# Optimization experiments

Measured on AMD Instinct MI355X. Metric: run time of the kernel, lower is better.

Reference implementation:

```python
import jax, jax.numpy as jnp
import numpy as np

B, C, V, K, H, W = 1, 3, 9, 8, 512, 512


def setup_inputs() -> dict:
    key = jax.random.key(0)
    k0, k1 = jax.random.split(key, 2)
    x = jax.random.normal(k0, (B, C, K, H, W), jnp.float32)          # FDL layers (spatial)
    y_views = jax.random.normal(k1, (B, C, V, H, W), jnp.float32)    # observed views (spatial)
    g = jnp.arange(3, dtype=jnp.float32) - 1.0                       # 3x3 camera grid positions
    uu, vv = jnp.meshgrid(g, g, indexing='ij')
    u = uu.reshape(-1)
    v = vv.reshape(-1)
    d = jnp.linspace(-2.0, 2.0, K).astype(jnp.float32)               # d_fdl disparities
    rho = jnp.full((1,), 0.3, jnp.float32)
    return {"x": x, "y_views": y_views, "u": u, "v": v, "d": d, "rho": rho}


def _pack_half_spectrum(Xf, x_c, y_c, n_proc):
    # [..., H, W] -> transpose to [..., W, H], center-roll so zero freq is at (x_c-1, y_c-1),
    # flatten x-major, keep the non-redundant half spectrum (first n_proc entries).
    Xt = jnp.swapaxes(Xf, -1, -2)
    Xt = jnp.roll(Xt, shift=(x_c - 1, y_c - 1), axis=(-2, -1))
    sh = Xt.shape
    return Xt.reshape(sh[:-2] + (sh[-2] * sh[-1],))[..., :n_proc]


def reference(x, y_views, u, v, d, rho):
    Bn, Cn, Kn = x.shape[0], x.shape[1], x.shape[2]
    Hn, Wn = x.shape[-2], x.shape[-1]
    rho = rho.reshape(())
    x_c = (Wn + 2) // 2                      # ceil((W+1)/2)
    y_c = (Hn + 2) // 2
    n_proc = Hn * (x_c - 1) + y_c            # half-spectrum size
    e0 = 1 - Hn % 2
    e1 = 1 - Wn % 2

    X = jnp.fft.fft2(x)                      # [B,C,K,H,W] complex64
    Y = jnp.fft.fft2(y_views)                # [B,C,V,H,W] complex64
    Xp = jnp.moveaxis(_pack_half_spectrum(X, x_c, y_c, n_proc), 2, 3) * rho   # [B,C,F,K]
    Yp = jnp.moveaxis(_pack_half_spectrum(Y, x_c, y_c, n_proc), 2, 3)         # [B,C,F,V]

    # centered angular frequency grids, flattened x-major to match packing order
    wx = (jnp.arange(Wn, dtype=jnp.float32) - (x_c - 1)) * (2.0 * np.pi / Wn)
    wy = (jnp.arange(Hn, dtype=jnp.float32) - (y_c - 1)) * (2.0 * np.pi / Hn)
    wx_f = jnp.repeat(wx, Hn)[:n_proc]       # [F]
    wy_f = jnp.tile(wy, Wn)[:n_proc]         # [F]

    # FDL data matrix A[f,v,k] = exp(i * d_k * (u_v*wx_f + v_v*wy_f))
    shift = u[None, :] * wx_f[:, None] + v[None, :] * wy_f[:, None]   # [F,V]
    A = jnp.exp(1j * shift[:, :, None] * d[None, None, :])            # [F,V,K] complex64
    Ah = jnp.conj(A)
    ATA = jnp.einsum('fvk,fvl->fkl', Ah, A)                           # [F,K,K]
    ATb = jnp.einsum('fvk,bcfv->bcfk', Ah, Yp)                        # [B,C,F,K]
    M = ATA + rho * jnp.eye(Kn, dtype=ATA.dtype)
    fdl = jnp.linalg.solve(M, (ATb + Xp)[..., None])[..., 0]          # [B,C,F,K]

    # pad redundant half with zeros, restore [B,C,K,H,W] layout
    fdl = jnp.pad(fdl, ((0, 0), (0, 0), (0, Hn * Wn - n_proc), (0, 0)))
    fdl = fdl.reshape(Bn, Cn, Wn, Hn, Kn).transpose(0, 1, 4, 3, 2)    # [B,C,K,H,W]

    # Hermitian (conjugate) symmetry reconstruction
    fdl = fdl.at[..., y_c:, x_c - 1:].set(jnp.conj(fdl[..., e0:y_c - 1, e1:x_c][..., ::-1, ::-1]))
    fdl = fdl.at[..., e0:y_c, x_c:].set(jnp.conj(fdl[..., y_c - 1:, e1:x_c - 1][..., ::-1, ::-1]))
    fdl = jnp.roll(fdl, shift=(1 - y_c, 1 - x_c), axis=(-2, -1))
    return jnp.fft.ifft2(fdl).real
```

## Files before the change

### kernel.cpp

```cpp
#include <hip/hip_runtime.h>
#include <math.h>

constexpr int N    = 512;
constexpr int LOGN = 9;
constexpr int NN   = N * N;
constexpr int CCH  = 3;
constexpr int KK   = 8;
constexpr int VV   = 9;
constexpr int FHALF = N * (N / 2) + (N / 2 + 1);
constexpr int NS   = 257;
constexpr float PI_F = 3.14159265358979323846f;

__device__ __forceinline__ float2 cmulf(float2 a, float2 b) {
    return make_float2(a.x * b.x - a.y * b.y, a.x * b.y + a.y * b.x);
}
__device__ __forceinline__ float2 cadd(float2 a, float2 b) { return make_float2(a.x + b.x, a.y + b.y); }
__device__ __forceinline__ float2 csub(float2 a, float2 b) { return make_float2(a.x - b.x, a.y - b.y); }

template<int SG>
__device__ __forceinline__ float2 cmuli(float2 z) {
    return (SG < 0) ? make_float2(z.y, -z.x) : make_float2(-z.y, z.x);
}

template<int SG>
__device__ __forceinline__ void dft8(float2 x[8]) {
    const float c = 0.70710678118654752440f;
    float2 a0 = cadd(x[0], x[4]), a1 = cadd(x[1], x[5]);
    float2 a2 = cadd(x[2], x[6]), a3 = cadd(x[3], x[7]);
    float2 d0 = csub(x[0], x[4]), d1 = csub(x[1], x[5]);
    float2 d2 = csub(x[2], x[6]), d3 = csub(x[3], x[7]);
    float2 b0 = d0;
    float2 b1 = cmulf(d1, make_float2(c, (float)SG * c));
    float2 b2 = cmuli<SG>(d2);
    float2 b3 = cmulf(d3, make_float2(-c, (float)SG * c));
    float2 aa0 = cadd(a0, a2), aa1 = cadd(a1, a3);
    float2 ab0 = csub(a0, a2), ab1 = cmuli<SG>(csub(a1, a3));
    float2 ba0 = cadd(b0, b2), ba1 = cadd(b1, b3);
    float2 bb0 = csub(b0, b2), bb1 = cmuli<SG>(csub(b1, b3));
    x[0] = cadd(aa0, aa1); x[4] = csub(aa0, aa1);
    x[2] = cadd(ab0, ab1); x[6] = csub(ab0, ab1);
    x[1] = cadd(ba0, ba1); x[5] = csub(ba0, ba1);
    x[3] = cadd(bb0, bb1); x[7] = csub(bb0, bb1);
}

__device__ __forceinline__ void twiddle8(float2 v[8], float base) {
    float sn, cs;
    __sincosf(base, &sn, &cs);
    float2 w1 = make_float2(cs, sn);
    float2 wk = w1;
    v[1] = cmulf(v[1], wk);
    #pragma unroll
    for (int k = 2; k < 8; ++k) { wk = cmulf(wk, w1); v[k] = cmulf(v[k], wk); }
}

template<int SG>
__device__ __forceinline__ void wave_fft512(float2 v[8], float* sre, float* sim,
                                            int t, int stride, int off) {
    int t1 = t >> 3, t0 = t & 7;
    dft8<SG>(v);
    twiddle8(v, (float)SG * (2.0f * PI_F / 512.0f) * (float)t);
    #pragma unroll
    for (int k = 0; k < 8; ++k) {
        int a = (68 * k + 8 * t1 + t0) * stride + off;
        sre[a] = v[k].x; sim[a] = v[k].y;
    }
    #pragma unroll
    for (int n = 0; n < 8; ++n) {
        int a = (68 * t1 + 8 * n + t0) * stride + off;
        v[n] = make_float2(sre[a], sim[a]);
    }
    dft8<SG>(v);
    twiddle8(v, (float)SG * (2.0f * PI_F / 64.0f) * (float)t0);
    #pragma unroll
    for (int k = 0; k < 8; ++k) {
        int a = (68 * t0 + 8 * k + t1) * stride + off;
        sre[a] = v[k].x; sim[a] = v[k].y;
    }
    #pragma unroll
    for (int n = 0; n < 8; ++n) {
        int a = (68 * n + 8 * t0 + t1) * stride + off;
        v[n] = make_float2(sre[a], sim[a]);
    }
    dft8<SG>(v);
}

__global__ __launch_bounds__(256) void k_fft_r2c_rows_pack_T(const float* __restrict__ inx,
                                                             const float* __restrict__ iny,
                                                             int nximg,
                                                             float2* __restrict__ outT) {
    __shared__ float ure[2313];
    __shared__ float uim[2313];
    int w = threadIdx.x >> 6, t = threadIdx.x & 63;
    int blk = blockIdx.x;
    int img = blk >> 6;
    int rowbase = (blk & 63) << 3;
    long long row0 = (long long)blk * 8 + 2 * w;
    long long xrows = (long long)nximg * N;
    const float* src0 = (row0 < xrows) ? (inx + row0 * N)
                                       : (iny + (row0 - xrows) * N);
    const float* src1 = src0 + N;
    float* sre = ure + w * 544;
    float* sim = uim + w * 544;
    float2 v[8];
    #pragma unroll
    for (int e = 0; e < 8; ++e) v[e] = make_float2(src0[t + 64 * e], src1[t + 64 * e]);
    wave_fft512<-1>(v, sre, sim, t, 1, 0);
    int kb = (t >> 3) + 8 * (t & 7);
    #pragma unroll
    for (int k0 = 0; k0 < 8; ++k0) {
        int p = kb + 64 * k0;
        sre[p] = v[k0].x; sim[p] = v[k0].y;
    }
    float2 r0v[4], r1v[4];
    #pragma unroll
    for (int k0 = 4; k0 < 8; ++k0) {
        int p  = kb + 64 * k0;
        int mp = 512 - p;
        float zmx = sre[mp], zmy = sim[mp];
        float2 Zp = v[k0];
        r0v[k0 - 4] = make_float2(0.5f * (Zp.x + zmx), 0.5f * (Zp.y - zmy));
        r1v[k0 - 4] = make_float2(0.5f * (Zp.y + zmy), 0.5f * (zmx - Zp.x));
    }
    float2 z0 = v[0];
    __syncthreads();
    #pragma unroll
    for (int k0 = 0; k0 < 4; ++k0) {
        int s = kb + 64 * k0;
        ure[s * 9 + 2 * w]     = r0v[k0].x; uim[s * 9 + 2 * w]     = r0v[k0].y;
        ure[s * 9 + 2 * w + 1] = r1v[k0].x; uim[s * 9 + 2 * w + 1] = r1v[k0].y;
    }
    if (t == 0) {
        ure[256 * 9 + 2 * w]     = z0.x; uim[256 * 9 + 2 * w]     = 0.0f;
        ure[256 * 9 + 2 * w + 1] = z0.y; uim[256 * 9 + 2 * w + 1] = 0.0f;
    }
    __syncthreads();
    float2* dst = outT + (long long)img * ((long long)NS * N);
    int tt = threadIdx.x;
    int r = tt & 7;
    #pragma unroll
    for (int j = 0; j < 8; ++j) {
        int s = j * 32 + (tt >> 3);
        dst[s * N + rowbase + r] = make_float2(ure[s * 9 + r], uim[s * 9 + r]);
    }
    if (tt < 8)
        dst[256 * N + rowbase + tt] = make_float2(ure[256 * 9 + tt], uim[256 * 9 + tt]);
}

__global__ __launch_bounds__(256) void k_fft_r2c_rows(const float* __restrict__ in,
                                                      float2* __restrict__ out) {
    __shared__ float sre[4][544];
    __shared__ float sim[4][544];
    int w = threadIdx.x >> 6, t = threadIdx.x & 63;
    long long grow = (long long)blockIdx.x * 4 + w;
    const float* src = in + grow * N;
    float2 v[8];
    #pragma unroll
    for (int e = 0; e < 8; ++e) v[e] = make_float2(src[t + 64 * e], 0.0f);
    wave_fft512<-1>(v, sre[w], sim[w], t, 1, 0);
    float2* dst = out + grow * N;
    int kb = (t >> 3) + 8 * (t & 7);
    #pragma unroll
    for (int k0 = 0; k0 < 8; ++k0) dst[kb + 64 * k0] = v[k0];
}

template<int SG>
__global__ __launch_bounds__(256) void k_fft_pairswap(float2* __restrict__ data,
                                                      float scale, int lex, int sex) {
    __shared__ float sre[4][544];
    __shared__ float sim[4][544];
    int w = threadIdx.x >> 6, t = threadIdx.x & 63;
    int b = blockIdx.x;
    long long imgBase = (long long)(b >> 7) * NN;
    int pa = (b & 127) << 1;
    int rowg = pa + (w & 1) + ((w >> 1) << 8);
    const float2* src = data + imgBase + (long long)rowg * N;
    float2 v[8];
    #pragma unroll
    for (int e = 0; e < 8; ++e) v[e] = src[t + 64 * (e ^ lex)];
    __syncthreads();
    wave_fft512<SG>(v, sre[w], sim[w], t, 1, 0);
    float2* dst = data + imgBase + (long long)(rowg ^ 256) * N;
    int kb = (t >> 3) + 8 * (t & 7);
    #pragma unroll
    for (int k0 = 0; k0 < 8; ++k0) {
        float2 z = v[k0];
        dst[kb + 64 * (k0 ^ sex)] = make_float2(z.x * scale, z.y * scale);
    }
}

__device__ __forceinline__ void accum_pair(float2 bacc[KK], float tr[KK], float s,
                                           float d0, float dlt, float2 Yp, float2 Yn) {
    float2 Sp = make_float2(Yp.x + Yn.x, Yp.y + Yn.y);
    float2 Dm = make_float2(Yp.x - Yn.x, Yp.y - Yn.y);
    float sn, cs;
    __sincosf(s * d0, &sn, &cs);  float2 p = make_float2(cs, sn);
    __sincosf(s * dlt, &sn, &cs); float2 q = make_float2(cs, sn);
    float2 w = q;
    #pragma unroll
    for (int k = 0; k < KK; ++k) {
        bacc[k].x += p.x * Sp.x + p.y * Dm.y;
        bacc[k].y += p.x * Sp.y - p.y * Dm.x;
        if (k < KK - 1) {
            p = cmulf(p, q);
            tr[k + 1] += 2.0f * w.x;
            w = cmulf(w, q);
        }
    }
}

__device__ __forceinline__ void solve_point(float2 bacc[KK], float tr[KK], float rho) {
    float diag = tr[0] + rho;
    float L[36], Li[KK];
    #pragma unroll
    for (int j = 0; j < KK; ++j) {
        float acc = diag;
        #pragma unroll
        for (int t = 0; t < j; ++t) { float l = L[(j * (j - 1)) / 2 + t]; acc -= l * l; }
        float dj = sqrtf(acc);
        float inv = 1.0f / dj;
        Li[j] = inv;
        #pragma unroll
        for (int i = j + 1; i < KK; ++i) {
            float a = tr[i - j];
            #pragma unroll
            for (int t = 0; t < j; ++t)
                a -= L[(i * (i - 1)) / 2 + t] * L[(j * (j - 1)) / 2 + t];
            L[(i * (i - 1)) / 2 + j] = a * inv;
        }
    }
    #pragma unroll
    for (int i = 0; i < KK; ++i) {
        float2 a = bacc[i];
        #pragma unroll
        for (int t = 0; t < i; ++t) {
            float l = L[(i * (i - 1)) / 2 + t];
            a.x -= l * bacc[t].x;
            a.y -= l * bacc[t].y;
        }
        bacc[i] = make_float2(a.x * Li[i], a.y * Li[i]);
    }
    #pragma unroll
    for (int i = KK - 1; i >= 0; --i) {
        float2 a = bacc[i];
        #pragma unroll
        for (int t = i + 1; t < KK; ++t) {
            float l = L[(t * (t - 1)) / 2 + i];
            a.x -= l * bacc[t].x;
            a.y -= l * bacc[t].y;
        }
        bacc[i] = make_float2(a.x * Li[i], a.y * Li[i]);
    }
}

__global__ __launch_bounds__(256) void k_fused_solve(const float2* __restrict__ Rt,
                                                     float2* __restrict__ P,
                                                     float2* __restrict__ S0,
                                                     int nximg,
                                                     const float* __restrict__ uu,
                                                     const float* __restrict__ vvp,
                                                     const float* __restrict__ dd,
                                                     const float* __restrict__ rhop) {
    __shared__ float2 buf[VV][N];
    __shared__ float fsre[4][544];
    __shared__ float fsim[4][544];
    int a  = blockIdx.x;
    int ch = blockIdx.y;
    int t  = threadIdx.x;
    int w = t >> 6, lane = t & 63;
    int kb = (lane >> 3) + 8 * (lane & 7);
    const long long LN = (long long)NS * N;

    {
        int ybase = nximg + ch * VV;
        #pragma unroll
        for (int rep = 0; rep < 3; ++rep) {
            int vimg = w + 4 * rep;
            if (vimg < VV) {
                const float2* src = Rt + (long long)(ybase + vimg) * LN + (long long)a * N;
                float2 fv[8];
                #pragma unroll
                for (int e = 0; e < 8; ++e) fv[e] = src[lane + 64 * e];
                wave_fft512<-1>(fv, fsre[w], fsim[w], lane, 1, 0);
                #pragma unroll
                for (int k0 = 0; k0 < 8; ++k0)
                    buf[vimg][kb + 64 * (k0 ^ 4)] = fv[k0];
            }
        }
    }
    __syncthreads();

    float rho = rhop[0];
    float d0 = dd[0], dlt = dd[1] - dd[0];
    const float C = 2.0f * PI_F / (float)N;
    float wxv = (float)(a - 256) * C;
    float wy0 = (float)(t - 256) * C;
    float wy1 = (float)(t)       * C;
    float2 bacc0[KK], bacc1[KK];
    float tr0[KK], tr1[KK];
    {
        float2 yc0 = buf[4][t], yc1 = buf[4][t + 256];
        #pragma unroll
        for (int k = 0; k < KK; ++k) { bacc0[k] = yc0; bacc1[k] = yc1; }
        tr0[0] = tr1[0] = (float)VV;
        #pragma unroll
        for (int l = 1; l < KK; ++l) { tr0[l] = 1.0f; tr1[l] = 1.0f; }
    }
    #pragma unroll
    for (int j = 0; j < 4; ++j) {
        int vp = 5 + j, vn = 3 - j;
        float su = uu[vp], sv = vvp[vp];
        float2 Yp0 = buf[vp][t],       Yn0 = buf[vn][t];
        float2 Yp1 = buf[vp][t + 256], Yn1 = buf[vn][t + 256];
        accum_pair(bacc0, tr0, su * wxv + sv * wy0, d0, dlt, Yp0, Yn0);
        accum_pair(bacc1, tr1, su * wxv + sv * wy1, d0, dlt, Yp1, Yn1);
    }
    __syncthreads();

    #pragma unroll
    for (int r = 0; r < 2; ++r) {
        int k = (w << 1) | r;
        const float2* src = Rt + (long long)(ch * KK + k) * LN + (long long)a * N;
        float2 fv[8];
        #pragma unroll
        for (int e = 0; e < 8; ++e) fv[e] = src[lane + 64 * e];
        wave_fft512<-1>(fv, fsre[w], fsim[w], lane, 1, 0);
        #pragma unroll
        for (int k0 = 0; k0 < 8; ++k0)
            buf[k][kb + 64 * (k0 ^ 4)] = fv[k0];
    }
    __syncthreads();

    #pragma unroll
    for (int k = 0; k < KK; ++k) {
        float2 x0v = buf[k][t], x1v = buf[k][t + 256];
        bacc0[k].x += rho * x0v.x; bacc0[k].y += rho * x0v.y;
        bacc1[k].x += rho * x1v.x; bacc1[k].y += rho * x1v.y;
    }
    solve_point(bacc0, tr0, rho);
    solve_point(bacc1, tr1, rho);
    #pragma unroll
    for (int k = 0; k < KK; ++k) {
        buf[k][t]       = bacc0[k];
        buf[k][t + 256] = bacc1[k];
    }
    __syncthreads();
    if (a == 256 && t >= 1) {
        int b = t + 256, bs = 256 - t;
        #pragma unroll
        for (int k = 0; k < KK; ++k) {
            float2 z = buf[k][bs];
            buf[k][b] = make_float2(z.x, -z.y);
        }
    }
    __syncthreads();

    const float inv512 = 1.0f / 512.0f;
    #pragma unroll
    for (int r = 0; r < 2; ++r) {
        int k = (w << 1) | r;
        float2 v[8];
        #pragma unroll
        for (int e = 0; e < 8; ++e)
            v[e] = buf[k][(lane + 64 * e) ^ 256];
        wave_fft512<1>(v, fsre[w], fsim[w], lane, 1, 0);
        float2 s0 = buf[k][0];
        if (lane == 0)
            S0[(long long)(ch * KK + k) * 257 + a] =
                make_float2(s0.x * inv512, s0.y * inv512);
        float2* Pimg = P + (long long)(ch * KK + k) * NN;
        int prow = (a >= 1 && a <= 255) ? (a + 256) : (a == 0 ? 256 : 0);
        float2* pmain = Pimg + (long long)prow * N;
        #pragma unroll
        for (int k0 = 0; k0 < 8; ++k0) {
            int pos = kb + 64 * k0;
            float2 W = v[k0];
            pmain[pos] = make_float2(W.x * inv512, W.y * inv512);
        }
    }
}

__global__ __launch_bounds__(256) void k_fft_cols_inv_real(const float2* __restrict__ in,
                                                           const float2* __restrict__ T0,
                                                           float* __restrict__ out,
                                                           float scale) {
    __shared__ float tre[4896];
    __shared__ float tim[4896];
    int t = threadIdx.x;
    long long imgOff = (long long)blockIdx.y * NN;
    int b0 = blockIdx.x << 3;
    {
        int xi2 = (t & 3) << 1;
        int yb  = t >> 2;
        const float2* img = in + imgOff;
        const float2* T0i = T0 + (long long)blockIdx.y * 257;
        #pragma unroll
        for (int it = 0; it < 4; ++it) {
            int p = 256 + it * 64 + yb;
            float4 q = *(const float4*)&img[(long long)p * N + b0 + xi2];
            int c = p * 9 + xi2;
            tre[c] = q.x; tim[c] = q.y; tre[c + 1] = q.z; tim[c + 1] = q.w;
            if (p > 256) {
                float2 t0 = T0i[p - 256];
                int m0 = b0 + xi2;
                float sg0 = (m0 & 1) ? -1.0f : 1.0f;
                float sg1 = -sg0;
                int cm = (512 - p) * 9 + xi2;
                tre[cm]     = q.x - t0.x * sg0;
                tim[cm]     = -q.y + t0.y * sg0;
                tre[cm + 1] = q.z - t0.x * sg1;
                tim[cm + 1] = -q.w + t0.y * sg1;
            }
        }
        if (t < 4) {
            int xi2b = t << 1;
            float4 q = *(const float4*)&img[(long long)(b0 + xi2b)];
            tre[xi2b] = q.x; tim[xi2b] = q.y; tre[xi2b + 1] = q.z; tim[xi2b + 1] = q.w;
        }
    }
    __syncthreads();
    int w = t >> 6, lane = t & 63;
    int kb = (lane >> 3) + 8 * (lane & 7);
    #pragma unroll
    for (int r = 0; r < 2; ++r) {
        int cc = (w << 1) | r;
        float2 v[8];
        #pragma unroll
        for (int e = 0; e < 8; ++e) {
            int a = (lane + 64 * e) * 9 + cc;
            v[e] = make_float2(tre[a], tim[a]);
        }
        wave_fft512<1>(v, tre, tim, lane, 9, cc);
        #pragma unroll
        for (int k0 = 0; k0 < 8; ++k0)
            tre[(kb + 64 * k0) * 9 + cc] = v[k0].x;
    }
    __syncthreads();
    {
        int xi = t >> 5, co = t & 31;
        float* orow = out + (long long)blockIdx.y * NN + (long long)(b0 + xi) * N;
        #pragma unroll
        for (int it = 0; it < 4; ++it) {
            int ww = it * 128 + co * 4;
            *(float4*)&orow[ww] = make_float4(tre[ww * 9 + xi] * scale,
                                              tre[(ww + 1) * 9 + xi] * scale,
                                              tre[(ww + 2) * 9 + xi] * scale,
                                              tre[(ww + 3) * 9 + xi] * scale);
        }
    }
}

__global__ __launch_bounds__(256) void k_transpose_inplace(float2* __restrict__ data) {
    int ti = blockIdx.x, tj = blockIdx.y;
    if (ti > tj) return;
    float2* img = data + (long long)blockIdx.z * NN;
    __shared__ float2 ta[32][33];
    __shared__ float2 tb[32][33];
    int tx = threadIdx.x, ty = threadIdx.y;
    int r0 = ti << 5, c0 = tj << 5;
    bool diag = (ti == tj);
    #pragma unroll
    for (int kk = 0; kk < 4; ++kk) {
        int r = ty + (kk << 3);
        ta[r][tx] = img[(long long)(r0 + r) * N + (c0 + tx)];
        if (!diag) tb[r][tx] = img[(long long)(c0 + r) * N + (r0 + tx)];
    }
    __syncthreads();
    #pragma unroll
    for (int kk = 0; kk < 4; ++kk) {
        int r = ty + (kk << 3);
        img[(long long)(c0 + r) * N + (r0 + tx)] = ta[tx][r];
        if (!diag) img[(long long)(r0 + r) * N + (c0 + tx)] = tb[tx][r];
    }
}

__global__ __launch_bounds__(256) void k_fft_c2r_rows(const float2* __restrict__ in,
                                                      float* __restrict__ out, float scale) {
    __shared__ float sre[4][544];
    __shared__ float sim[4][544];
    int w = threadIdx.x >> 6, t = threadIdx.x & 63;
    long long grow = (long long)blockIdx.x * 4 + w;
    const float2* src = in + grow * N;
    float2 v[8];
    #pragma unroll
    for (int e = 0; e < 8; ++e) v[e] = src[t + 64 * e];
    wave_fft512<1>(v, sre[w], sim[w], t, 1, 0);
    float* dst = out + grow * N;
    int kb = (t >> 3) + 8 * (t & 7);
    #pragma unroll
    for (int k0 = 0; k0 < 8; ++k0) dst[kb + 64 * k0] = v[k0].x * scale;
}

__global__ __launch_bounds__(256) void k_solve(float2* __restrict__ Xs,
                                               const float2* __restrict__ Ys,
                                               const float* __restrict__ uu,
                                               const float* __restrict__ vv,
                                               const float* __restrict__ dd,
                                               const float* __restrict__ rhop) {
    int f = blockIdx.x * 256 + threadIdx.x;
    if (f >= FHALF) return;
    long long coffX = (long long)blockIdx.y * KK * NN;
    long long coffY = (long long)blockIdx.y * VV * NN;
    float rho = rhop[0];
    int x = f >> LOGN;
    int y = f & (N - 1);
    float wxv = (float)(x - N / 2) * (2.0f * PI_F / (float)N);
    float wyv = (float)(y - N / 2) * (2.0f * PI_F / (float)N);
    float d0 = dd[0], dlt = dd[1] - dd[0];
    float2 bacc[KK];
    float tr[KK];
    {
        float2 Yc = Ys[coffY + (long long)4 * NN + f];
        #pragma unroll
        for (int k = 0; k < KK; ++k) bacc[k] = Yc;
        tr[0] = (float)VV;
        #pragma unroll
        for (int l = 1; l < KK; ++l) tr[l] = 1.0f;
    }
    #pragma unroll
    for (int j = 0; j < 4; ++j) {
        int vp = 5 + j, vn = 3 - j;
        float s = uu[vp] * wxv + vv[vp] * wyv;
        accum_pair(bacc, tr, s, d0, dlt,
                   Ys[coffY + (long long)vp * NN + f],
                   Ys[coffY + (long long)vn * NN + f]);
    }
    #pragma unroll
    for (int k = 0; k < KK; ++k) {
        float2 Xk = Xs[coffX + (long long)k * NN + f];
        bacc[k].x += rho * Xk.x;
        bacc[k].y += rho * Xk.y;
    }
    solve_point(bacc, tr, rho);
    int xm = (N - x) & (N - 1);
    int ym = (N - y) & (N - 1);
    long long fm = (long long)xm * N + ym;
    bool conjMirror = false, zeroMirror = false;
    if (x >= 1 && x <= N / 2 - 1) {
        if (y == 0) zeroMirror = true; else conjMirror = true;
    } else if (x == N / 2 && y >= 1 && y <= N / 2 - 1) {
        conjMirror = true;
    }
    #pragma unroll
    for (int k = 0; k < KK; ++k) {
        float2* base = Xs + coffX + (long long)k * NN;
        float2 z = bacc[k];
        base[f] = z;
        if (conjMirror)      base[fm] = make_float2(z.x, -z.y);
        else if (zeroMirror) base[fm] = make_float2(0.f, 0.f);
    }
}

extern "C" void kernel_launch(void* const* d_in, const int* in_sizes, int n_in,
                              void* d_out, int out_size, void* d_ws, size_t ws_size,
                              hipStream_t stream) {
    (void)in_sizes; (void)n_in; (void)out_size;
    const float* x   = (const float*)d_in[0];
    const float* yv  = (const float*)d_in[1];
    const float* uu  = (const float*)d_in[2];
    const float* vvp = (const float*)d_in[3];
    const float* dd  = (const float*)d_in[4];
    const float* rho = (const float*)d_in[5];
    float* out = (float*)d_out;
    float2* ws = (float2*)d_ws;

    const float invN = 1.0f / (float)N;
    const size_t lnPer = (size_t)NS * N;
    const size_t needBatched =
        ((size_t)CCH * (KK + VV) * lnPer + (size_t)CCH * KK * NN
         + (size_t)CCH * KK * 257) * sizeof(float2);
    const size_t needChan =
        ((size_t)(KK + VV) * lnPer + (size_t)KK * NN
         + (size_t)KK * 257) * sizeof(float2);

    if (ws_size >= needChan) {
        bool batched = ws_size >= needBatched;
        int iters = batched ? 1 : CCH;
        int ncs   = batched ? CCH : 1;
        int nx = ncs * KK, ny = ncs * VV;
        for (int it = 0; it < iters; ++it) {
            float2* Rt = ws;
            float2* P  = ws + (size_t)(nx + ny) * lnPer;
            float2* S0 = P  + (size_t)nx * NN;
            const float* xin = x  + (size_t)it * KK * NN;
            const float* yin = yv + (size_t)it * VV * NN;
            float* oout = out + (size_t)it * KK * NN;
            k_fft_r2c_rows_pack_T<<<(nx + ny) * 64, 256, 0, stream>>>(xin, yin, nx, Rt);
            k_fused_solve<<<dim3(257, ncs), 256, 0, stream>>>(Rt, P, S0, nx,
                                                              uu, vvp, dd, rho);
            k_fft_cols_inv_real<<<dim3(N / 8, nx), 256, 0, stream>>>(P, S0, oout, invN);
        }
    } else {
        for (int it = 0; it < CCH; ++it) {
            float2* Xb = ws;
            float2* Yb = ws + (size_t)KK * NN;
            const float* xin = x  + (size_t)it * KK * NN;
            const float* yin = yv + (size_t)it * VV * NN;
            float* oout = out + (size_t)it * KK * NN;
            k_fft_r2c_rows<<<KK * (N / 4), 256, 0, stream>>>(xin, Xb);
            k_fft_r2c_rows<<<VV * (N / 4), 256, 0, stream>>>(yin, Yb);
            k_transpose_inplace<<<dim3(16, 16, KK), dim3(32, 8), 0, stream>>>(Xb);
            k_transpose_inplace<<<dim3(16, 16, VV), dim3(32, 8), 0, stream>>>(Yb);
            k_fft_pairswap<-1><<<KK * (N / 4), 256, 0, stream>>>(Xb, 1.0f, 0, 4);
            k_fft_pairswap<-1><<<VV * (N / 4), 256, 0, stream>>>(Yb, 1.0f, 0, 4);
            k_solve<<<dim3((FHALF + 255) / 256, 1), 256, 0, stream>>>(Xb, Yb, uu, vvp, dd, rho);
            k_fft_pairswap<1><<<KK * (N / 4), 256, 0, stream>>>(Xb, invN, 4, 0);
            k_transpose_inplace<<<dim3(16, 16, KK), dim3(32, 8), 0, stream>>>(Xb);
            k_fft_c2r_rows<<<KK * (N / 4), 256, 0, stream>>>(Xb, oout, invN);
        }
    }
}
```

Measured before the change: 181.2 us.

## Use 512 threads per fused-solve block with split re/im shared buffers

The fused solve kernel now launches 512 threads per block, so each thread handles a single frequency point instead of two and each wave runs one FFT instead of two. The shared memory is reorganised into separate padded real/imag planes per image, and the FFTs use those rows directly as scratch instead of a separate per-wave scratch area. This halves the per-thread register state and serial work, which gives more parallelism per column, at the cost of a larger block and higher register pressure under launch_bounds(512,4). The in-place FFT scratch reuse also needs the row data to be read out before the transform overwrites it.

```diff
diff --git a/kernel.cpp b/kernel.cpp
--- a/kernel.cpp
+++ b/kernel.cpp
@@ -9,6 +9,7 @@
 constexpr int VV   = 9;
 constexpr int FHALF = N * (N / 2) + (N / 2 + 1);
 constexpr int NS   = 257;
+constexpr int RW   = 544;
 constexpr float PI_F = 3.14159265358979323846f;
 
 __device__ __forceinline__ float2 cmulf(float2 a, float2 b) {
@@ -252,17 +253,16 @@
     }
 }
 
-__global__ __launch_bounds__(256) void k_fused_solve(const float2* __restrict__ Rt,
-                                                     float2* __restrict__ P,
-                                                     float2* __restrict__ S0,
-                                                     int nximg,
-                                                     const float* __restrict__ uu,
-                                                     const float* __restrict__ vvp,
-                                                     const float* __restrict__ dd,
-                                                     const float* __restrict__ rhop) {
-    __shared__ float2 buf[VV][N];
-    __shared__ float fsre[4][544];
-    __shared__ float fsim[4][544];
+__global__ __launch_bounds__(512, 4) void k_fused_solve(const float2* __restrict__ Rt,
+                                                        float2* __restrict__ P,
+                                                        float2* __restrict__ S0,
+                                                        int nximg,
+                                                        const float* __restrict__ uu,
+                                                        const float* __restrict__ vvp,
+                                                        const float* __restrict__ dd,
+                                                        const float* __restrict__ rhop) {
+    __shared__ float bre[VV][RW];
+    __shared__ float bim[VV][RW];
     int a  = blockIdx.x;
     int ch = blockIdx.y;
     int t  = threadIdx.x;
@@ -273,17 +273,19 @@
     {
         int ybase = nximg + ch * VV;
         #pragma unroll
-        for (int rep = 0; rep < 3; ++rep) {
-            int vimg = w + 4 * rep;
+        for (int rep = 0; rep < 2; ++rep) {
+            int vimg = w + 8 * rep;
             if (vimg < VV) {
                 const float2* src = Rt + (long long)(ybase + vimg) * LN + (long long)a * N;
                 float2 fv[8];
                 #pragma unroll
                 for (int e = 0; e < 8; ++e) fv[e] = src[lane + 64 * e];
-                wave_fft512<-1>(fv, fsre[w], fsim[w], lane, 1, 0);
+                wave_fft512<-1>(fv, bre[vimg], bim[vimg], lane, 1, 0);
                 #pragma unroll
-                for (int k0 = 0; k0 < 8; ++k0)
-                    buf[vimg][kb + 64 * (k0 ^ 4)] = fv[k0];
+                for (int k0 = 0; k0 < 8; ++k0) {
+                    int pos = kb + 64 * (k0 ^ 4);
+                    bre[vimg][pos] = fv[k0].x; bim[vimg][pos] = fv[k0].y;
+                }
             }
         }
     }
@@ -293,80 +295,76 @@
     float d0 = dd[0], dlt = dd[1] - dd[0];
     const float C = 2.0f * PI_F / (float)N;
     float wxv = (float)(a - 256) * C;
-    float wy0 = (float)(t - 256) * C;
-    float wy1 = (float)(t)       * C;
-    float2 bacc0[KK], bacc1[KK];
-    float tr0[KK], tr1[KK];
+    float wy  = (float)(t - 256) * C;
+    float2 bacc[KK];
+    float tr[KK];
     {
-        float2 yc0 = buf[4][t], yc1 = buf[4][t + 256];
-        #pragma unroll
-        for (int k = 0; k < KK; ++k) { bacc0[k] = yc0; bacc1[k] = yc1; }
-        tr0[0] = tr1[0] = (float)VV;
-        #pragma unroll
-        for (int l = 1; l < KK; ++l) { tr0[l] = 1.0f; tr1[l] = 1.0f; }
+        float2 yc = make_float2(bre[4][t], bim[4][t]);
+        #pragma unroll
+        for (int k = 0; k < KK; ++k) bacc[k] = yc;
+        tr[0] = (float)VV;
+        #pragma unroll
+        for (int l = 1; l < KK; ++l) tr[l] = 1.0f;
     }
     #pragma unroll
     for (int j = 0; j < 4; ++j) {
         int vp = 5 + j, vn = 3 - j;
-        float su = uu[vp], sv = vvp[vp];
-        float2 Yp0 = buf[vp][t],       Yn0 = buf[vn][t];
-        float2 Yp1 = buf[vp][t + 256], Yn1 = buf[vn][t + 256];
-        accum_pair(bacc0, tr0, su * wxv + sv * wy0, d0, dlt, Yp0, Yn0);
-        accum_pair(bacc1, tr1, su * wxv + sv * wy1, d0, dlt, Yp1, Yn1);
-    }
-    __syncthreads();
-
-    #pragma unroll
-    for (int r = 0; r < 2; ++r) {
-        int k = (w << 1) | r;
-        const float2* src = Rt + (long long)(ch * KK + k) * LN + (long long)a * N;
+        accum_pair(bacc, tr, uu[vp] * wxv + vvp[vp] * wy, d0, dlt,
+                   make_float2(bre[vp][t], bim[vp][t]),
+                   make_float2(bre[vn][t], bim[vn][t]));
+    }
+    __syncthreads();
+
+    {
+        const float2* src = Rt + (long long)(ch * KK + w) * LN + (long long)a * N;
         float2 fv[8];
         #pragma unroll
         for (int e = 0; e < 8; ++e) fv[e] = src[lane + 64 * e];
-        wave_fft512<-1>(fv, fsre[w], fsim[w], lane, 1, 0);
-        #pragma unroll
-        for (int k0 = 0; k0 < 8; ++k0)
-            buf[k][kb + 64 * (k0 ^ 4)] = fv[k0];
+        wave_fft512<-1>(fv, bre[w], bim[w], lane, 1, 0);
+        #pragma unroll
+        for (int k0 = 0; k0 < 8; ++k0) {
+            int pos = kb + 64 * (k0 ^ 4);
+            bre[w][pos] = fv[k0].x; bim[w][pos] = fv[k0].y;
+        }
     }
     __syncthreads();
 
     #pragma unroll
     for (int k = 0; k < KK; ++k) {
-        float2 x0v = buf[k][t], x1v = buf[k][t + 256];
-        bacc0[k].x += rho * x0v.x; bacc0[k].y += rho * x0v.y;
-        bacc1[k].x += rho * x1v.x; bacc1[k].y += rho * x1v.y;
-    }
-    solve_point(bacc0, tr0, rho);
-    solve_point(bacc1, tr1, rho);
+        bacc[k].x += rho * bre[k][t];
+        bacc[k].y += rho * bim[k][t];
+    }
+    solve_point(bacc, tr, rho);
     #pragma unroll
     for (int k = 0; k < KK; ++k) {
-        buf[k][t]       = bacc0[k];
-        buf[k][t + 256] = bacc1[k];
-    }
-    __syncthreads();
-    if (a == 256 && t >= 1) {
-        int b = t + 256, bs = 256 - t;
+        bre[k][t] = bacc[k].x;
+        bim[k][t] = bacc[k].y;
+    }
+    __syncthreads();
+    if (a == 256 && t >= 257) {
+        int bs = 512 - t;
         #pragma unroll
         for (int k = 0; k < KK; ++k) {
-            float2 z = buf[k][bs];
-            buf[k][b] = make_float2(z.x, -z.y);
-        }
-    }
-    __syncthreads();
-
-    const float inv512 = 1.0f / 512.0f;
-    #pragma unroll
-    for (int r = 0; r < 2; ++r) {
-        int k = (w << 1) | r;
+            bre[k][t] = bre[k][bs];
+            bim[k][t] = -bim[k][bs];
+        }
+    }
+    __syncthreads();
+
+    {
+        const float inv512 = 1.0f / 512.0f;
+        int k = w;
         float2 v[8];
         #pragma unroll
-        for (int e = 0; e < 8; ++e)
-            v[e] = buf[k][(lane + 64 * e) ^ 256];
-        wave_fft512<1>(v, fsre[w], fsim[w], lane, 1, 0);
-        float2 s0 = buf[k][0];
+        for (int e = 0; e < 8; ++e) {
+            int idx = (lane + 64 * e) ^ 256;
+            v[e] = make_float2(bre[k][idx], bim[k][idx]);
+        }
+        float s0x = bre[k][0], s0y = bim[k][0];
+        wave_fft512<1>(v, bre[k], bim[k], lane, 1, 0);
         if (lane == 0)
             S0[(long long)(ch * KK + k) * 257 + a] =
-                make_float2(s0.x * inv512, s0.y * inv512);
+                make_float2(s0x * inv512, s0y * inv512);
         float2* Pimg = P + (long long)(ch * KK + k) * NN;
         int prow = (a >= 1 && a <= 255) ? (a + 256) : (a == 0 ? 256 : 0);
         float2* pmain = Pimg + (long long)prow * N;
@@ -585,7 +583,7 @@
             const float* yin = yv + (size_t)it * VV * NN;
             float* oout = out + (size_t)it * KK * NN;
             k_fft_r2c_rows_pack_T<<<(nx + ny) * 64, 256, 0, stream>>>(xin, yin, nx, Rt);
-            k_fused_solve<<<dim3(257, ncs), 256, 0, stream>>>(Rt, P, S0, nx,
+            k_fused_solve<<<dim3(257, ncs), 512, 0, stream>>>(Rt, P, S0, nx,
                                                               uu, vvp, dd, rho);
             k_fft_cols_inv_real<<<dim3(N / 8, nx), 256, 0, stream>>>(P, S0, oout, invN);
         }
```

After: 160.2 us. 1.13x faster.
